# Optimization experiments

Measured on AMD Instinct MI355X. Metric: run time of the kernel, lower is better.

## Reference

```python
import math
import jax, jax.numpy as jnp
import numpy as np

DIM = 2048
HID = 4 * DIM
SEQ = 2048
BATCH = 2
EPS = 1e-5


def _layernorm(x, g, b):
    mu = jnp.mean(x, axis=-1, keepdims=True)
    var = jnp.var(x, axis=-1, keepdims=True)
    return (x - mu) * jax.lax.rsqrt(var + EPS) * g + b


def setup_inputs() -> dict:
    key = jax.random.key(0)
    ks = jax.random.split(key, 12)
    s = 1.0 / math.sqrt(DIM)
    x = jax.random.normal(ks[0], (BATCH, SEQ, DIM), dtype=jnp.float32)
    # additive causal mask: 0 on/below diagonal, -1e9 above
    mask = jnp.where(jnp.tril(jnp.ones((SEQ, SEQ), dtype=bool)), 0.0, -1e9).astype(jnp.float32)
    freqs_cis = jax.random.normal(ks[1], (SEQ, 64), dtype=jnp.float32)  # unused by forward
    return {
        "x": x,
        "mask": mask,
        "start_pos": 0,
        "freqs_cis": freqs_cis,
        "wq": jax.random.normal(ks[2], (DIM, DIM), dtype=jnp.float32) * s,
        "bq": jnp.zeros((DIM,), dtype=jnp.float32),
        "wk": jax.random.normal(ks[3], (DIM, DIM), dtype=jnp.float32) * s,
        "bk": jnp.zeros((DIM,), dtype=jnp.float32),
        "wv": jax.random.normal(ks[4], (DIM, DIM), dtype=jnp.float32) * s,
        "bv": jnp.zeros((DIM,), dtype=jnp.float32),
        "g_ln1": jnp.ones((DIM,), dtype=jnp.float32),
        "b_ln1": jnp.zeros((DIM,), dtype=jnp.float32),
        "g_ln2": jnp.ones((DIM,), dtype=jnp.float32),
        "b_ln2": jnp.zeros((DIM,), dtype=jnp.float32),
        "w1": jax.random.normal(ks[5], (DIM, HID), dtype=jnp.float32) * s,
        "b1": jnp.zeros((HID,), dtype=jnp.float32),
        "w2": jax.random.normal(ks[6], (HID, DIM), dtype=jnp.float32) * (1.0 / math.sqrt(HID)),
        "b2": jnp.zeros((DIM,), dtype=jnp.float32),
    }


def reference(x, mask, start_pos, freqs_cis, wq, bq, wk, bk, wv, bv,
              g_ln1, b_ln1, g_ln2, b_ln2, w1, b1, w2, b2):
    # pre-norm attention (no head split; scale by sqrt(full dim); dropout=eval identity)
    h = _layernorm(x, g_ln1, b_ln1)
    q = h @ wq + bq
    k = h @ wk + bk
    v = h @ wv + bv
    scores = jnp.einsum('bqd,bkd->bqk', q, k) / math.sqrt(DIM) + mask
    attn = jax.nn.softmax(scores, axis=-1)
    attn_out = jnp.einsum('bqk,bkd->bqd', attn, v)
    h2 = _layernorm(x + attn_out, g_ln2, b_ln2)
    ffn = jax.nn.gelu(h2 @ w1 + b1, approximate=False) @ w2 + b2
    # NOTE: original code adds FFN output to the ORIGINAL x (attn residual dropped here)
    return x + ffn
```

## Files before the change

### kernel.cpp

```cpp
#include <hip/hip_runtime.h>
#include <math.h>

#define DIM_ 2048
#define HID_ 8192
#define SEQ_ 2048
#define BATCH_ 2
#define TOK_ (BATCH_*SEQ_)

typedef __attribute__((ext_vector_type(4))) float f32x4;
typedef __attribute__((ext_vector_type(8))) __bf16 bf16x8;
typedef __attribute__((ext_vector_type(4))) unsigned int u32x4;
typedef __attribute__((ext_vector_type(4))) short s16x4;
typedef __attribute__((ext_vector_type(8))) short s16x8;
typedef __attribute__((address_space(3))) short* lds_sp;

__device__ __forceinline__ short f2bf(float f) {
  union { float f; unsigned u; } v; v.f = f;
  unsigned r = v.u + 0x7FFFu + ((v.u >> 16) & 1u);
  return (short)(r >> 16);
}
__device__ __forceinline__ float bf2f(short s) {
  union { unsigned u; float f; } v; v.u = ((unsigned)(unsigned short)s) << 16;
  return v.f;
}

__device__ __forceinline__ f32x4 mfma16(u32x4 a, u32x4 b, f32x4 c) {
  return __builtin_amdgcn_mfma_f32_16x16x32_bf16(
      __builtin_bit_cast(bf16x8, a), __builtin_bit_cast(bf16x8, b), c, 0, 0, 0);
}

#define DSR(dst, addr) asm volatile("ds_read_b128 %0, %1" : "=v"(dst) : "v"(addr))
#define BARv()  __builtin_amdgcn_s_barrier()
#define LGKMW(n) do { asm volatile("s_waitcnt lgkmcnt(" #n ")" ::: "memory"); \
                      __builtin_amdgcn_sched_barrier(0); } while(0)
#define VM3()   asm volatile("s_waitcnt vmcnt(3)" ::: "memory")
#define VM4()   asm volatile("s_waitcnt vmcnt(4)" ::: "memory")
#define PRIO1() __builtin_amdgcn_s_setprio(1)
#define PRIO0() __builtin_amdgcn_s_setprio(0)
#define AS1 const __attribute__((address_space(1))) void*
#define AS3 __attribute__((address_space(3))) void*

#define TILE_MAP(BM, BN) \
  const int nwg  = gridDim.x * gridDim.y; \
  const int orig = blockIdx.y * gridDim.x + blockIdx.x; \
  const int wgid = (orig & 7) * (nwg >> 3) + (orig >> 3); \
  const int gy4  = (int)gridDim.y << 2; \
  const int rem  = wgid % gy4; \
  const int tn   = ((wgid / gy4) * 4 + (rem & 3)) * (BN); \
  const int tm   = (rem >> 2) * (BM);

template<int EPI>
__device__ __forceinline__ void epi_store(void* Cv, const float* bias, const float* aux,
                                          int z, long long sC, int ldc, int N,
                                          int row, int col, float v)
{
  if (EPI == 1) {
    ((float*)Cv + (long long)z * sC)[(long long)row * ldc + col] = v;
  } else if (EPI == 0) {
    v += bias[col];
    ((short*)Cv + (long long)z * sC)[(long long)row * ldc + col] = f2bf(v);
  } else if (EPI == 2) {
    v += bias[col];
    v = 0.5f * v * (1.0f + erff(v * 0.70710678118654752f));
    ((short*)Cv + (long long)z * sC)[(long long)row * ldc + col] = f2bf(v);
  } else if (EPI == 3) {
    v += bias[col] + aux[(long long)row * ldc + col];
    ((float*)Cv + (long long)z * sC)[(long long)row * ldc + col] = v;
  } else {
    v = v * 0.022097086912079608f + aux[(long long)row * ldc + col];
    ((short*)Cv + (long long)z * sC)[(long long)row * ldc + col] = f2bf(v);
  }
}

#define G256_RD1(slot) do { \
  const unsigned s_ = (unsigned)(slot)*16384u; \
  DSR(af[0], aRd + s_);          DSR(af[1], aRd + s_ + 1024u); \
  DSR(af[2], aRd + s_ + 2048u);  DSR(af[3], aRd + s_ + 3072u); \
  DSR(af[4], aRd + s_ + 4096u);  DSR(af[5], aRd + s_ + 5120u); \
  DSR(af[6], aRd + s_ + 6144u);  DSR(af[7], aRd + s_ + 7168u); \
  DSR(bf0[0], bRd + s_);         DSR(bf0[1], bRd + s_ + 1024u); \
} while(0)

#define G256_RD2(slot) do { \
  const unsigned s_ = (unsigned)(slot)*16384u; \
  DSR(bf1[0], bRd + s_ + 2048u); DSR(bf1[1], bRd + s_ + 3072u); \
} while(0)

#define G256_MM(c0, bA, bB) do { \
  _Pragma("unroll") \
  for (int fr_ = 0; fr_ < 8; ++fr_) { \
    acc[fr_][(c0)]   = mfma16(af[fr_], bA, acc[fr_][(c0)]); \
    acc[fr_][(c0)+1] = mfma16(af[fr_], bB, acc[fr_][(c0)+1]); \
  } \
} while(0)

template<int EPI>
__global__ __launch_bounds__(512, 2)
void gemm256(const short* __restrict__ A, const short* __restrict__ B,
             void* __restrict__ Cv, const float* __restrict__ bias,
             const float* __restrict__ aux,
             int M, int N, int K, int lda, int ldb, int ldc,
             long long sA, long long sB, long long sC)
{
  __shared__ __align__(16) short As[3*256*32];
  __shared__ __align__(16) short Bs[3*256*32];
  const int lane = threadIdx.x & 63;
  const int wave = threadIdx.x >> 6;
  const int wr = wave >> 2, wc = wave & 3;
  TILE_MAP(256, 256)
  const int z = blockIdx.z;
  A += (long long)z * sA;
  B += (long long)z * sB;

  const int NT = K >> 5;

  const int rr   = wave * 16 + (lane >> 2);
  const int soff = (((lane & 3) ^ ((lane >> 3) & 3)) << 3);
  const short* pA = A + (long long)(tm + rr) * lda + soff;
  const short* pB = B + (long long)(tn + rr) * ldb + soff;
  const long long lda128 = 128LL * lda;
  const long long ldb128 = 128LL * ldb;

  auto stA = [&](int t, int slot) {
    const long long ko = (long long)t << 5;
    __builtin_amdgcn_global_load_lds((AS1)(pA + ko),
        (AS3)(As + slot * 8192 + wave * 512), 16, 0, 0);
    __builtin_amdgcn_global_load_lds((AS1)(pA + lda128 + ko),
        (AS3)(As + slot * 8192 + 4096 + wave * 512), 16, 0, 0);
  };
  auto stB = [&](int t, int slot) {
    const long long ko = (long long)t << 5;
    __builtin_amdgcn_global_load_lds((AS1)(pB + ko),
        (AS3)(Bs + slot * 8192 + wave * 512), 16, 0, 0);
    __builtin_amdgcn_global_load_lds((AS1)(pB + ldb128 + ko),
        (AS3)(Bs + slot * 8192 + 4096 + wave * 512), 16, 0, 0);
  };

  const unsigned asB = (unsigned)(unsigned long long)(lds_sp)As;
  const unsigned bsB = (unsigned)(unsigned long long)(lds_sp)Bs;
  const int l15 = lane & 15, l4 = lane >> 4;
  const unsigned offk = (unsigned)((l4 ^ ((l15 >> 1) & 3)) << 4);
  const unsigned aRd = asB + (unsigned)((wr * 128 + l15) * 64) + offk;
  const unsigned bRd = bsB + (unsigned)((wc * 64 + l15) * 64) + offk;

  f32x4 acc[8][4] = {};
  u32x4 af[8], bf0[2], bf1[2];

  stA(0, 0); stB(0, 0);
  stA(1 < NT ? 1 : 0, 1); stB(1 < NT ? 1 : 0, 1);
  VM4();
  BARv();

  int rd = 0;
  #pragma unroll 1
  for (int t = 0; t < NT; ++t) {
    const int st = rd + 2 >= 3 ? rd - 1 : rd + 2;
    const int tc = t + 2 < NT ? t + 2 : NT - 1;
    G256_RD1(rd);
    G256_RD2(rd);
    stA(tc, st); stB(tc, st);
    LGKMW(2);
    PRIO1(); G256_MM(0, bf0[0], bf0[1]);
    LGKMW(0);
    G256_MM(2, bf1[0], bf1[1]); PRIO0();
    VM4();
    BARv();
    rd = rd + 1 >= 3 ? 0 : rd + 1;
  }

  const int row0 = tm + wr * 128 + l4 * 4;
  const int col0 = tn + wc * 64 + l15;
  #pragma unroll
  for (int fr = 0; fr < 8; ++fr)
    #pragma unroll
    for (int j = 0; j < 4; ++j)
      #pragma unroll
      for (int fc = 0; fc < 4; ++fc)
        epi_store<EPI>(Cv, bias, aux, z, sC, ldc, N,
                       row0 + fr * 16 + j, col0 + fc * 16, acc[fr][fc][j]);
}

template<int EPI>
__global__ __launch_bounds__(512, 2)
void gemm_bn128(const short* __restrict__ A, const short* __restrict__ B,
                void* __restrict__ Cv, const float* __restrict__ bias,
                const float* __restrict__ aux,
                int M, int N, int K, int lda, int ldb, int ldc,
                long long sA, long long sB, long long sC)
{
  __shared__ __align__(16) short As[3*256*32];
  __shared__ __align__(16) short Bs[3*256*32];
  const int lane = threadIdx.x & 63;
  const int wave = threadIdx.x >> 6;
  const int wr = wave >> 2, wc = wave & 3;
  TILE_MAP(256, 128)
  const int z = blockIdx.z;
  A += (long long)z * sA;
  B += (long long)z * sB;

  const int NT = K >> 5;

  const int rr   = wave * 16 + (lane >> 2);
  const int soff = (((lane & 3) ^ ((lane >> 3) & 3)) << 3);
  const short* pA = A + (long long)(tm + rr) * lda + soff;
  const short* pB = B + (long long)(tn + rr) * ldb + soff;
  const long long lda128 = 128LL * lda;

  auto stage = [&](int t, int slot) {
    const long long ko = (long long)t << 5;
    __builtin_amdgcn_global_load_lds((AS1)(pA + ko),
        (AS3)(As + slot * 8192 + wave * 512), 16, 0, 0);
    __builtin_amdgcn_global_load_lds((AS1)(pA + lda128 + ko),
        (AS3)(As + slot * 8192 + 4096 + wave * 512), 16, 0, 0);
    __builtin_amdgcn_global_load_lds((AS1)(pB + ko),
        (AS3)(Bs + slot * 8192 + wave * 512), 16, 0, 0);
  };

  const unsigned asB = (unsigned)(unsigned long long)(lds_sp)As;
  const unsigned bsB = (unsigned)(unsigned long long)(lds_sp)Bs;
  const int l15 = lane & 15, l4 = lane >> 4;
  const unsigned offk = (unsigned)((l4 ^ ((l15 >> 1) & 3)) << 4);
  const unsigned aRd = asB + (unsigned)((wr * 128 + l15) * 64) + offk;
  const unsigned bRd = bsB + (unsigned)((wc * 32 + l15) * 64) + offk;

  f32x4 acc[8][2] = {};
  u32x4 af[8], bf[2];

  stage(0, 0);
  stage(1 < NT ? 1 : 0, 1);
  VM3();
  BARv();

  int rd = 0;
  #pragma unroll 1
  for (int t = 0; t < NT; ++t) {
    const int st = rd + 2 >= 3 ? rd - 1 : rd + 2;
    const int tc = t + 2 < NT ? t + 2 : NT - 1;
    {
      const unsigned s_ = (unsigned)rd * 16384u;
      DSR(bf[0], bRd + s_);          DSR(bf[1], bRd + s_ + 1024u);
      DSR(af[0], aRd + s_);          DSR(af[1], aRd + s_ + 1024u);
      DSR(af[2], aRd + s_ + 2048u);  DSR(af[3], aRd + s_ + 3072u);
      DSR(af[4], aRd + s_ + 4096u);  DSR(af[5], aRd + s_ + 5120u);
      DSR(af[6], aRd + s_ + 6144u);  DSR(af[7], aRd + s_ + 7168u);
    }
    stage(tc, st);
    LGKMW(4);
    PRIO1();
    #pragma unroll
    for (int fr = 0; fr < 4; ++fr) {
      acc[fr][0] = mfma16(af[fr], bf[0], acc[fr][0]);
      acc[fr][1] = mfma16(af[fr], bf[1], acc[fr][1]);
    }
    LGKMW(0);
    #pragma unroll
    for (int fr = 4; fr < 8; ++fr) {
      acc[fr][0] = mfma16(af[fr], bf[0], acc[fr][0]);
      acc[fr][1] = mfma16(af[fr], bf[1], acc[fr][1]);
    }
    PRIO0();
    VM3();
    BARv();
    rd = rd + 1 >= 3 ? 0 : rd + 1;
  }

  const int row0 = tm + wr * 128 + l4 * 4;
  const int col0 = tn + wc * 32 + l15;
  #pragma unroll
  for (int fr = 0; fr < 8; ++fr)
    #pragma unroll
    for (int j = 0; j < 4; ++j)
      #pragma unroll
      for (int fc = 0; fc < 2; ++fc)
        epi_store<EPI>(Cv, bias, aux, z, sC, ldc, N,
                       row0 + fr * 16 + j, col0 + fc * 16, acc[fr][fc][j]);
}

#define HRD2(slot) do { \
  const unsigned a_ = aBaseH + (unsigned)(slot)*8192u; \
  const unsigned b_ = bBaseH + (unsigned)(slot)*16384u; \
  DSR(bf[0], b_ + offk);          DSR(bf[1], b_ + 1024u + offk); \
  DSR(bf[2], b_ + 2048u + offk);  DSR(bf[3], b_ + 3072u + offk); \
  DSR(af[0], a_ + offk);          DSR(af[1], a_ + 1024u + offk); \
  DSR(af[2], a_ + 2048u + offk);  DSR(af[3], a_ + 3072u + offk); \
} while(0)

#define HROW(mi) do { \
  _Pragma("unroll") \
  for (int ni = 0; ni < 4; ++ni) \
    acc[mi][ni] = mfma16(af[mi], bf[ni], acc[mi][ni]); \
} while(0)

template<int EPI, int CZ>
__global__ __launch_bounds__(512, 4)
void gemm_hi(const short* __restrict__ A, const short* __restrict__ B,
             void* __restrict__ Cv, const float* __restrict__ bias,
             const float* __restrict__ aux,
             int M, int N, int K, int lda, int ldb, int ldc,
             long long sA, long long sB, long long sC)
{
  __shared__ __align__(16) short As[3*128*32];
  __shared__ __align__(16) short Bs[3*256*32];
  const int lane = threadIdx.x & 63;
  const int wave = threadIdx.x >> 6;
  const int wr = wave >> 2, wc = wave & 3;
  TILE_MAP(128, 256)
  if (CZ == 1 && tn >= tm + 128) return;
  const int z = blockIdx.z;
  A += (long long)z * sA;
  B += (long long)z * sB;

  const int NT = (CZ == 2) ? ((tm + 128) >> 5) : (K >> 5);

  const int rr   = wave * 16 + (lane >> 2);
  const int soff = (((lane & 3) ^ ((lane >> 3) & 3)) << 3);
  const short* pA = A + (long long)(tm + rr) * lda + soff;
  const short* pB = B + (long long)(tn + rr) * ldb + soff;
  const long long ldb128 = 128LL * ldb;

  auto stage = [&](int t, int slot) {
    const long long ko = (long long)t << 5;
    __builtin_amdgcn_global_load_lds((AS1)(pA + ko),
        (AS3)(As + slot * 4096 + wave * 512), 16, 0, 0);
    __builtin_amdgcn_global_load_lds((AS1)(pB + ko),
        (AS3)(Bs + slot * 8192 + wave * 512), 16, 0, 0);
    __builtin_amdgcn_global_load_lds((AS1)(pB + ldb128 + ko),
        (AS3)(Bs + slot * 8192 + 4096 + wave * 512), 16, 0, 0);
  };

  const unsigned asB = (unsigned)(unsigned long long)(lds_sp)As;
  const unsigned bsB = (unsigned)(unsigned long long)(lds_sp)Bs;
  const int l15 = lane & 15, l4 = lane >> 4;
  const unsigned offk  = (unsigned)((l4 ^ ((l15 >> 1) & 3)) << 4);
  const unsigned aBaseH = asB + (unsigned)(wr * 4096 + l15 * 64);
  const unsigned bBaseH = bsB + (unsigned)(wc * 4096 + l15 * 64);

  f32x4 acc[4][4] = {};
  u32x4 af[4], bf[4];

  stage(0, 0);
  stage(1 < NT ? 1 : 0, 1);
  VM3();
  BARv();

  int rd = 0;
  #pragma unroll 1
  for (int t = 0; t < NT; ++t) {
    const int st = rd + 2 >= 3 ? rd - 1 : rd + 2;
    const int tc = t + 2 < NT ? t + 2 : NT - 1;
    HRD2(rd);
    stage(tc, st);
    LGKMW(3);
    PRIO1(); HROW(0);
    LGKMW(2); HROW(1);
    LGKMW(1); HROW(2);
    LGKMW(0); HROW(3); PRIO0();
    VM3();
    BARv();
    rd = rd + 1 >= 3 ? 0 : rd + 1;
  }

  const int row0 = tm + wr * 64 + l4 * 4;
  const int col0 = tn + wc * 64 + l15;
  #pragma unroll
  for (int mi = 0; mi < 4; ++mi)
    #pragma unroll
    for (int j = 0; j < 4; ++j)
      #pragma unroll
      for (int ni = 0; ni < 4; ++ni)
        epi_store<EPI>(Cv, bias, aux, z, sC, ldc, N,
                       row0 + mi * 16 + j, col0 + ni * 16, acc[mi][ni][j]);
}

__global__ __launch_bounds__(256)
void ln_kernel(const float* __restrict__ x, const float* __restrict__ res,
               const float* __restrict__ g, const float* __restrict__ b,
               short* __restrict__ out, int hasres)
{
  const int row = blockIdx.x;
  const int tid = threadIdx.x;
  const float4* X = (const float4*)x + (long long)row * 512;
  float4 v0 = X[tid], v1 = X[tid + 256];
  if (hasres) {
    const float4* R = (const float4*)res + (long long)row * 512;
    float4 r0 = R[tid], r1 = R[tid + 256];
    v0.x += r0.x; v0.y += r0.y; v0.z += r0.z; v0.w += r0.w;
    v1.x += r1.x; v1.y += r1.y; v1.z += r1.z; v1.w += r1.w;
  }
  float s1 = v0.x + v0.y + v0.z + v0.w + v1.x + v1.y + v1.z + v1.w;
  float s2 = v0.x*v0.x + v0.y*v0.y + v0.z*v0.z + v0.w*v0.w
           + v1.x*v1.x + v1.y*v1.y + v1.z*v1.z + v1.w*v1.w;
  #pragma unroll
  for (int o = 32; o > 0; o >>= 1) { s1 += __shfl_xor(s1, o); s2 += __shfl_xor(s2, o); }
  __shared__ float red[8];
  if ((tid & 63) == 0) { red[tid >> 6] = s1; red[4 + (tid >> 6)] = s2; }
  __syncthreads();
  s1 = red[0] + red[1] + red[2] + red[3];
  s2 = red[4] + red[5] + red[6] + red[7];
  const float mean = s1 * (1.0f / 2048.0f);
  const float var  = s2 * (1.0f / 2048.0f) - mean * mean;
  const float rstd = rsqrtf(var + 1e-5f);
  const float4* G  = (const float4*)g;
  const float4* Bb = (const float4*)b;
  float4 g0 = G[tid], g1 = G[tid + 256], b0 = Bb[tid], b1 = Bb[tid + 256];
  s16x4 o0, o1;
  o0[0] = f2bf((v0.x - mean) * rstd * g0.x + b0.x);
  o0[1] = f2bf((v0.y - mean) * rstd * g0.y + b0.y);
  o0[2] = f2bf((v0.z - mean) * rstd * g0.z + b0.z);
  o0[3] = f2bf((v0.w - mean) * rstd * g0.w + b0.w);
  o1[0] = f2bf((v1.x - mean) * rstd * g1.x + b1.x);
  o1[1] = f2bf((v1.y - mean) * rstd * g1.y + b1.y);
  o1[2] = f2bf((v1.z - mean) * rstd * g1.z + b1.z);
  o1[3] = f2bf((v1.w - mean) * rstd * g1.w + b1.w);
  *(s16x4*)&out[(long long)row * 2048 + tid * 4]        = o0;
  *(s16x4*)&out[(long long)row * 2048 + 1024 + tid * 4] = o1;
}

__global__ __launch_bounds__(256)
void softmax_causal_kernel(short* __restrict__ probs)
{
  const long long row = blockIdx.x;
  const int q  = blockIdx.x & (SEQ_ - 1);
  const int tid = threadIdx.x;
  short* P = probs + row * 2048 + tid * 8;
  const int kbase = tid * 8;
  s16x8 in = *(const s16x8*)P;
  float a[8];
  #pragma unroll
  for (int i = 0; i < 8; ++i) a[i] = bf2f(in[i]);
  float mx = -1e30f;
  #pragma unroll
  for (int i = 0; i < 8; ++i) {
    const float av = (kbase + i <= q) ? a[i] : -1e30f;
    mx = fmaxf(mx, av);
  }
  #pragma unroll
  for (int o = 32; o > 0; o >>= 1) mx = fmaxf(mx, __shfl_xor(mx, o));
  __shared__ float red[8];
  if ((tid & 63) == 0) red[tid >> 6] = mx;
  __syncthreads();
  mx = fmaxf(fmaxf(red[0], red[1]), fmaxf(red[2], red[3]));
  float e[8], sum = 0.f;
  #pragma unroll
  for (int i = 0; i < 8; ++i) {
    e[i] = (kbase + i <= q) ? __expf(a[i] - mx) : 0.f;
    sum += e[i];
  }
  #pragma unroll
  for (int o = 32; o > 0; o >>= 1) sum += __shfl_xor(sum, o);
  if ((tid & 63) == 0) red[4 + (tid >> 6)] = sum;
  __syncthreads();
  sum = red[4] + red[5] + red[6] + red[7];
  const float inv = 1.0f / sum;
  s16x8 o;
  #pragma unroll
  for (int i = 0; i < 8; ++i) o[i] = f2bf(e[i] * inv);
  *(s16x8*)P = o;
}

__global__ __launch_bounds__(256)
void cvt_transpose64(const float* __restrict__ in, short* __restrict__ out,
                     int R, int C)
{
  __shared__ float t[64][69];
  const int r0 = blockIdx.y << 6, c0 = blockIdx.x << 6;
  const int tx = threadIdx.x & 15, ty = threadIdx.x >> 4;
  #pragma unroll
  for (int p = 0; p < 4; ++p) {
    const int r = ty + p * 16;
    float4 v = *(const float4*)&in[(long long)(r0 + r) * C + c0 + tx * 4];
    t[r][tx*4+0] = v.x; t[r][tx*4+1] = v.y; t[r][tx*4+2] = v.z; t[r][tx*4+3] = v.w;
  }
  __syncthreads();
  #pragma unroll
  for (int p = 0; p < 4; ++p) {
    const int oc = ty + p * 16;
    s16x4 o;
    o[0] = f2bf(t[tx*4+0][oc]); o[1] = f2bf(t[tx*4+1][oc]);
    o[2] = f2bf(t[tx*4+2][oc]); o[3] = f2bf(t[tx*4+3][oc]);
    *(s16x4*)&out[(long long)(c0 + oc) * R + r0 + tx * 4] = o;
  }
}

__global__ __launch_bounds__(256)
void transpose_bf16_kernel(const short* __restrict__ in, short* __restrict__ out,
                           int ldin, int ldout, long long sin_, long long sout_)
{
  __shared__ short t[32][33];
  in  += (long long)blockIdx.z * sin_;
  out += (long long)blockIdx.z * sout_;
  const int tx = threadIdx.x & 31, ty = threadIdx.x >> 5;
  const int r0 = blockIdx.y << 5, c0 = blockIdx.x << 5;
  #pragma unroll
  for (int i = 0; i < 32; i += 8)
    t[ty + i][tx] = in[(long long)(r0 + ty + i) * ldin + c0 + tx];
  __syncthreads();
  #pragma unroll
  for (int i = 0; i < 32; i += 8)
    out[(long long)(c0 + ty + i) * ldout + r0 + tx] = t[tx][ty + i];
}

__global__ __launch_bounds__(256)
void concat_bias_kernel(const float* a, const float* b, const float* c, float* o)
{
  const int i = blockIdx.x * 256 + threadIdx.x;
  o[i] = i < 2048 ? a[i] : (i < 4096 ? b[i - 2048] : c[i - 4096]);
}

extern "C" void kernel_launch(void* const* d_in, const int* in_sizes, int n_in,
                              void* d_out, int out_size, void* d_ws, size_t ws_size,
                              hipStream_t stream)
{
  const float* x    = (const float*)d_in[0];
  const float* mask = (const float*)d_in[1];
  const float* wq   = (const float*)d_in[4];
  const float* bq   = (const float*)d_in[5];
  const float* wk   = (const float*)d_in[6];
  const float* bk   = (const float*)d_in[7];
  const float* wv   = (const float*)d_in[8];
  const float* bv   = (const float*)d_in[9];
  const float* g1   = (const float*)d_in[10];
  const float* b1   = (const float*)d_in[11];
  const float* g2   = (const float*)d_in[12];
  const float* b2   = (const float*)d_in[13];
  const float* w1   = (const float*)d_in[14];
  const float* bw1  = (const float*)d_in[15];
  const float* w2   = (const float*)d_in[16];
  const float* bw2  = (const float*)d_in[17];
  float* out = (float*)d_out;

  char* p = (char*)d_ws;
  auto take = [&](size_t bytes) { char* r = p; p += (bytes + 255) & ~(size_t)255; return r; };
  short* wqkvT = (short*)take((size_t)3 * DIM_ * DIM_ * 2);
  short* w1T   = (short*)take((size_t)DIM_ * HID_ * 2);
  short* w2T   = (short*)take((size_t)HID_ * DIM_ * 2);
  short* h_bf  = (short*)take((size_t)TOK_ * DIM_ * 2);
  short* qkv   = (short*)take((size_t)TOK_ * 3 * DIM_ * 2);
  short* vT    = (short*)take((size_t)BATCH_ * DIM_ * SEQ_ * 2);
  float* attno = (float*)take((size_t)TOK_ * DIM_ * 4);
  short* attn  = (short*)take((size_t)BATCH_ * SEQ_ * SEQ_ * 2);
  float* cbias = (float*)take((size_t)3 * DIM_ * 4);
  short* ffn1  = qkv;
  short* h2    = h_bf;

  const dim3 blk(256), gblk(512);
  cvt_transpose64<<<dim3(DIM_/64, DIM_/64), blk, 0, stream>>>(wq, wqkvT, DIM_, DIM_);
  cvt_transpose64<<<dim3(DIM_/64, DIM_/64), blk, 0, stream>>>(wk, wqkvT + (size_t)DIM_*DIM_, DIM_, DIM_);
  cvt_transpose64<<<dim3(DIM_/64, DIM_/64), blk, 0, stream>>>(wv, wqkvT + (size_t)2*DIM_*DIM_, DIM_, DIM_);
  cvt_transpose64<<<dim3(HID_/64, DIM_/64), blk, 0, stream>>>(w1, w1T, DIM_, HID_);
  cvt_transpose64<<<dim3(DIM_/64, HID_/64), blk, 0, stream>>>(w2, w2T, HID_, DIM_);
  concat_bias_kernel<<<24, blk, 0, stream>>>(bq, bk, bv, cbias);
  ln_kernel<<<TOK_, blk, 0, stream>>>(x, nullptr, g1, b1, h_bf, 0);
  gemm_bn128<0><<<dim3(6144/128, TOK_/256, 1), gblk, 0, stream>>>(
      h_bf, wqkvT, qkv, cbias, nullptr, TOK_, 6144, DIM_, DIM_, DIM_, 6144, 0, 0, 0);
  gemm_hi<4,1><<<dim3(SEQ_/256, SEQ_/128, BATCH_), gblk, 0, stream>>>(
      qkv, qkv + DIM_, attn, nullptr, mask, SEQ_, SEQ_, DIM_, 6144, 6144, SEQ_,
      (long long)SEQ_ * 6144, (long long)SEQ_ * 6144, (long long)SEQ_ * SEQ_);
  softmax_causal_kernel<<<BATCH_ * SEQ_, blk, 0, stream>>>(attn);
  transpose_bf16_kernel<<<dim3(DIM_/32, SEQ_/32, BATCH_), blk, 0, stream>>>(
      qkv + 2*DIM_, vT, 6144, SEQ_, (long long)SEQ_ * 6144, (long long)DIM_ * SEQ_);
  gemm_hi<1,2><<<dim3(DIM_/256, SEQ_/128, BATCH_), gblk, 0, stream>>>(
      attn, vT, attno, nullptr, nullptr, SEQ_, DIM_, SEQ_, SEQ_, SEQ_, DIM_,
      (long long)SEQ_ * SEQ_, (long long)DIM_ * SEQ_, (long long)SEQ_ * DIM_);
  ln_kernel<<<TOK_, blk, 0, stream>>>(x, attno, g2, b2, h2, 1);
  gemm256<2><<<dim3(HID_/256, TOK_/256, 1), gblk, 0, stream>>>(
      h2, w1T, ffn1, bw1, nullptr, TOK_, HID_, DIM_, DIM_, DIM_, HID_, 0, 0, 0);
  gemm_hi<3,0><<<dim3(DIM_/256, TOK_/128, 1), gblk, 0, stream>>>(
      ffn1, w2T, out, bw2, x, TOK_, DIM_, HID_, HID_, HID_, DIM_, 0, 0, 0);
}
```

Baseline: 621.8 us.

## Switch GEMMs to 4-slot double-tile pipeline, bf16 attention output, fused QKV weight convert

The gemm256 and gemm_bn128 kernels move from a 3-slot ring with a barrier per K-tile to a 4-slot ring that processes two K-tiles per barrier and waits on vmcnt(0). A new gemm_hi4 kernel uses the same scheme for the FFN down-projection. The attention-output GEMM now writes bf16 through a new epilogue, and layernorm 2 reads that bf16 residual, halving that buffer's traffic at some precision cost. The three Q/K/V weight conversion launches are merged into one 3D launch. Halving the barriers targets synchronisation overhead, but the larger LDS footprint and full vmcnt drains may reduce occupancy or overlap.

```diff
diff --git a/kernel.cpp b/kernel.cpp
--- a/kernel.cpp
+++ b/kernel.cpp
@@ -33,8 +33,8 @@
 #define BARv()  __builtin_amdgcn_s_barrier()
 #define LGKMW(n) do { asm volatile("s_waitcnt lgkmcnt(" #n ")" ::: "memory"); \
                       __builtin_amdgcn_sched_barrier(0); } while(0)
+#define VM0()   asm volatile("s_waitcnt vmcnt(0)" ::: "memory")
 #define VM3()   asm volatile("s_waitcnt vmcnt(3)" ::: "memory")
-#define VM4()   asm volatile("s_waitcnt vmcnt(4)" ::: "memory")
 #define PRIO1() __builtin_amdgcn_s_setprio(1)
 #define PRIO0() __builtin_amdgcn_s_setprio(0)
 #define AS1 const __attribute__((address_space(1))) void*
@@ -66,8 +66,10 @@
   } else if (EPI == 3) {
     v += bias[col] + aux[(long long)row * ldc + col];
     ((float*)Cv + (long long)z * sC)[(long long)row * ldc + col] = v;
+  } else if (EPI == 4) {
+    v = v * 0.022097086912079608f + aux[(long long)row * ldc + col];
+    ((short*)Cv + (long long)z * sC)[(long long)row * ldc + col] = f2bf(v);
   } else {
-    v = v * 0.022097086912079608f + aux[(long long)row * ldc + col];
     ((short*)Cv + (long long)z * sC)[(long long)row * ldc + col] = f2bf(v);
   }
 }
@@ -94,6 +96,15 @@
   } \
 } while(0)
 
+#define G256_TILE(slot, tt, sslot) do { \
+  G256_RD1(slot); G256_RD2(slot); \
+  stA(tt, sslot); stB(tt, sslot); \
+  LGKMW(2); \
+  PRIO1(); G256_MM(0, bf0[0], bf0[1]); \
+  LGKMW(0); \
+  G256_MM(2, bf1[0], bf1[1]); PRIO0(); \
+} while(0)
+
 template<int EPI>
 __global__ __launch_bounds__(512, 2)
 void gemm256(const short* __restrict__ A, const short* __restrict__ B,
@@ -102,8 +113,8 @@
              int M, int N, int K, int lda, int ldb, int ldc,
              long long sA, long long sB, long long sC)
 {
-  __shared__ __align__(16) short As[3*256*32];
-  __shared__ __align__(16) short Bs[3*256*32];
+  __shared__ __align__(16) short As[4*256*32];
+  __shared__ __align__(16) short Bs[4*256*32];
   const int lane = threadIdx.x & 63;
   const int wave = threadIdx.x >> 6;
   const int wr = wave >> 2, wc = wave & 3;
@@ -113,6 +124,7 @@
   B += (long long)z * sB;
 
   const int NT = K >> 5;
+  const int NW = NT >> 1;
 
   const int rr   = wave * 16 + (lane >> 2);
   const int soff = (((lane & 3) ^ ((lane >> 3) & 3)) << 3);
@@ -148,24 +160,20 @@
 
   stA(0, 0); stB(0, 0);
   stA(1 < NT ? 1 : 0, 1); stB(1 < NT ? 1 : 0, 1);
-  VM4();
+  VM0();
   BARv();
 
   int rd = 0;
   #pragma unroll 1
-  for (int t = 0; t < NT; ++t) {
-    const int st = rd + 2 >= 3 ? rd - 1 : rd + 2;
-    const int tc = t + 2 < NT ? t + 2 : NT - 1;
-    G256_RD1(rd);
-    G256_RD2(rd);
-    stA(tc, st); stB(tc, st);
-    LGKMW(2);
-    PRIO1(); G256_MM(0, bf0[0], bf0[1]);
-    LGKMW(0);
-    G256_MM(2, bf1[0], bf1[1]); PRIO0();
-    VM4();
+  for (int w = 0; w < NW; ++w) {
+    const int t2 = 2*w + 2 < NT ? 2*w + 2 : NT - 1;
+    const int t3 = 2*w + 3 < NT ? 2*w + 3 : NT - 1;
+    const int st = rd ^ 2;
+    G256_TILE(rd,     t2, st);
+    G256_TILE(rd + 1, t3, st + 1);
+    VM0();
     BARv();
-    rd = rd + 1 >= 3 ? 0 : rd + 1;
+    rd ^= 2;
   }
 
   const int row0 = tm + wr * 128 + l4 * 4;
@@ -180,6 +188,30 @@
                        row0 + fr * 16 + j, col0 + fc * 16, acc[fr][fc][j]);
 }
 
+#define BN128_TILE(slot, tt, sslot) do { \
+  const unsigned s_ = (unsigned)(slot)*16384u; \
+  DSR(bf[0], bRd + s_);          DSR(bf[1], bRd + s_ + 1024u); \
+  DSR(af[0], aRd + s_);          DSR(af[1], aRd + s_ + 1024u); \
+  DSR(af[2], aRd + s_ + 2048u);  DSR(af[3], aRd + s_ + 3072u); \
+  DSR(af[4], aRd + s_ + 4096u);  DSR(af[5], aRd + s_ + 5120u); \
+  DSR(af[6], aRd + s_ + 6144u);  DSR(af[7], aRd + s_ + 7168u); \
+  stage(tt, sslot); \
+  LGKMW(4); \
+  PRIO1(); \
+  _Pragma("unroll") \
+  for (int fr_ = 0; fr_ < 4; ++fr_) { \
+    acc[fr_][0] = mfma16(af[fr_], bf[0], acc[fr_][0]); \
+    acc[fr_][1] = mfma16(af[fr_], bf[1], acc[fr_][1]); \
+  } \
+  LGKMW(0); \
+  _Pragma("unroll") \
+  for (int fr_ = 4; fr_ < 8; ++fr_) { \
+    acc[fr_][0] = mfma16(af[fr_], bf[0], acc[fr_][0]); \
+    acc[fr_][1] = mfma16(af[fr_], bf[1], acc[fr_][1]); \
+  } \
+  PRIO0(); \
+} while(0)
+
 template<int EPI>
 __global__ __launch_bounds__(512, 2)
 void gemm_bn128(const short* __restrict__ A, const short* __restrict__ B,
@@ -188,8 +220,8 @@
                 int M, int N, int K, int lda, int ldb, int ldc,
                 long long sA, long long sB, long long sC)
 {
-  __shared__ __align__(16) short As[3*256*32];
-  __shared__ __align__(16) short Bs[3*256*32];
+  __shared__ __align__(16) short As[4*256*32];
+  __shared__ __align__(16) short Bs[4*128*32];
   const int lane = threadIdx.x & 63;
   const int wave = threadIdx.x >> 6;
   const int wr = wave >> 2, wc = wave & 3;
@@ -199,6 +231,7 @@
   B += (long long)z * sB;
 
   const int NT = K >> 5;
+  const int NW = NT >> 1;
 
   const int rr   = wave * 16 + (lane >> 2);
   const int soff = (((lane & 3) ^ ((lane >> 3) & 3)) << 3);
@@ -213,7 +246,7 @@
     __builtin_amdgcn_global_load_lds((AS1)(pA + lda128 + ko),
         (AS3)(As + slot * 8192 + 4096 + wave * 512), 16, 0, 0);
     __builtin_amdgcn_global_load_lds((AS1)(pB + ko),
-        (AS3)(Bs + slot * 8192 + wave * 512), 16, 0, 0);
+        (AS3)(Bs + slot * 4096 + wave * 512), 16, 0, 0);
   };
 
   const unsigned asB = (unsigned)(unsigned long long)(lds_sp)As;
@@ -221,47 +254,80 @@
   const int l15 = lane & 15, l4 = lane >> 4;
   const unsigned offk = (unsigned)((l4 ^ ((l15 >> 1) & 3)) << 4);
   const unsigned aRd = asB + (unsigned)((wr * 128 + l15) * 64) + offk;
-  const unsigned bRd = bsB + (unsigned)((wc * 32 + l15) * 64) + offk;
+  const unsigned bRd0 = bsB + (unsigned)((wc * 32 + l15) * 64) + offk;
 
   f32x4 acc[8][2] = {};
   u32x4 af[8], bf[2];
 
   stage(0, 0);
   stage(1 < NT ? 1 : 0, 1);
-  VM3();
+  VM0();
   BARv();
 
   int rd = 0;
   #pragma unroll 1
-  for (int t = 0; t < NT; ++t) {
-    const int st = rd + 2 >= 3 ? rd - 1 : rd + 2;
-    const int tc = t + 2 < NT ? t + 2 : NT - 1;
+  for (int w = 0; w < NW; ++w) {
+    const int t2 = 2*w + 2 < NT ? 2*w + 2 : NT - 1;
+    const int t3 = 2*w + 3 < NT ? 2*w + 3 : NT - 1;
+    const int st = rd ^ 2;
     {
-      const unsigned s_ = (unsigned)rd * 16384u;
-      DSR(bf[0], bRd + s_);          DSR(bf[1], bRd + s_ + 1024u);
-      DSR(af[0], aRd + s_);          DSR(af[1], aRd + s_ + 1024u);
-      DSR(af[2], aRd + s_ + 2048u);  DSR(af[3], aRd + s_ + 3072u);
-      DSR(af[4], aRd + s_ + 4096u);  DSR(af[5], aRd + s_ + 5120u);
-      DSR(af[6], aRd + s_ + 6144u);  DSR(af[7], aRd + s_ + 7168u);
+      const unsigned bRd = bRd0 - (unsigned)0;
+      {
+        const unsigned s_ = (unsigned)rd * 8192u;
+        DSR(bf[0], bRd0 + s_);          DSR(bf[1], bRd0 + s_ + 1024u);
+      }
+      {
+        const unsigned s_ = (unsigned)rd * 16384u;
+        DSR(af[0], aRd + s_);          DSR(af[1], aRd + s_ + 1024u);
+        DSR(af[2], aRd + s_ + 2048u);  DSR(af[3], aRd + s_ + 3072u);
+        DSR(af[4], aRd + s_ + 4096u);  DSR(af[5], aRd + s_ + 5120u);
+        DSR(af[6], aRd + s_ + 6144u);  DSR(af[7], aRd + s_ + 7168u);
+      }
+      stage(t2, st);
+      LGKMW(4);
+      PRIO1();
+      #pragma unroll
+      for (int fr = 0; fr < 4; ++fr) {
+        acc[fr][0] = mfma16(af[fr], bf[0], acc[fr][0]);
+        acc[fr][1] = mfma16(af[fr], bf[1], acc[fr][1]);
+      }
+      LGKMW(0);
+      #pragma unroll
+      for (int fr = 4; fr < 8; ++fr) {
+        acc[fr][0] = mfma16(af[fr], bf[0], acc[fr][0]);
+        acc[fr][1] = mfma16(af[fr], bf[1], acc[fr][1]);
+      }
+      PRIO0();
+      {
+        const unsigned s_ = (unsigned)(rd + 1) * 8192u;
+        DSR(bf[0], bRd0 + s_);          DSR(bf[1], bRd0 + s_ + 1024u);
+      }
+      {
+        const unsigned s_ = (unsigned)(rd + 1) * 16384u;
+        DSR(af[0], aRd + s_);          DSR(af[1], aRd + s_ + 1024u);
+        DSR(af[2], aRd + s_ + 2048u);  DSR(af[3], aRd + s_ + 3072u);
+        DSR(af[4], aRd + s_ + 4096u);  DSR(af[5], aRd + s_ + 5120u);
+        DSR(af[6], aRd + s_ + 6144u);  DSR(af[7], aRd + s_ + 7168u);
+      }
+      stage(t3, st + 1);
+      LGKMW(4);
+      PRIO1();
+      #pragma unroll
+      for (int fr = 0; fr < 4; ++fr) {
+        acc[fr][0] = mfma16(af[fr], bf[0], acc[fr][0]);
+        acc[fr][1] = mfma16(af[fr], bf[1], acc[fr][1]);
+      }
+      LGKMW(0);
+      #pragma unroll
+      for (int fr = 4; fr < 8; ++fr) {
+        acc[fr][0] = mfma16(af[fr], bf[0], acc[fr][0]);
+        acc[fr][1] = mfma16(af[fr], bf[1], acc[fr][1]);
+      }
+      PRIO0();
     }
-    stage(tc, st);
-    LGKMW(4);
-    PRIO1();
-    #pragma unroll
-    for (int fr = 0; fr < 4; ++fr) {
-      acc[fr][0] = mfma16(af[fr], bf[0], acc[fr][0]);
-      acc[fr][1] = mfma16(af[fr], bf[1], acc[fr][1]);
-    }
-    LGKMW(0);
-    #pragma unroll
-    for (int fr = 4; fr < 8; ++fr) {
-      acc[fr][0] = mfma16(af[fr], bf[0], acc[fr][0]);
-      acc[fr][1] = mfma16(af[fr], bf[1], acc[fr][1]);
-    }
-    PRIO0();
-    VM3();
+    VM0();
     BARv();
-    rd = rd + 1 >= 3 ? 0 : rd + 1;
+    rd ^= 2;
   }
 
   const int row0 = tm + wr * 128 + l4 * 4;
@@ -372,8 +438,100 @@
                        row0 + mi * 16 + j, col0 + ni * 16, acc[mi][ni][j]);
 }
 
+#define H4_TILE(slot, tt, sslot) do { \
+  const unsigned a_ = aBaseH + (unsigned)(slot)*8192u; \
+  const unsigned b_ = bBaseH + (unsigned)(slot)*16384u; \
+  DSR(bf[0], b_ + offk);          DSR(bf[1], b_ + 1024u + offk); \
+  DSR(bf[2], b_ + 2048u + offk);  DSR(bf[3], b_ + 3072u + offk); \
+  DSR(af[0], a_ + offk);          DSR(af[1], a_ + 1024u + offk); \
+  DSR(af[2], a_ + 2048u + offk);  DSR(af[3], a_ + 3072u + offk); \
+  stage(tt, sslot); \
+  LGKMW(3); \
+  PRIO1(); HROW(0); \
+  LGKMW(2); HROW(1); \
+  LGKMW(1); HROW(2); \
+  LGKMW(0); HROW(3); PRIO0(); \
+} while(0)
+
+template<int EPI>
+__global__ __launch_bounds__(512, 2)
+void gemm_hi4(const short* __restrict__ A, const short* __restrict__ B,
+              void* __restrict__ Cv, const float* __restrict__ bias,
+              const float* __restrict__ aux,
+              int M, int N, int K, int lda, int ldb, int ldc,
+              long long sA, long long sB, long long sC)
+{
+  __shared__ __align__(16) short As[4*128*32];
+  __shared__ __align__(16) short Bs[4*256*32];
+  const int lane = threadIdx.x & 63;
+  const int wave = threadIdx.x >> 6;
+  const int wr = wave >> 2, wc = wave & 3;
+  TILE_MAP(128, 256)
+  const int z = blockIdx.z;
+  A += (long long)z * sA;
+  B += (long long)z * sB;
+
+  const int NT = K >> 5;
+  const int NW = NT >> 1;
+
+  const int rr   = wave * 16 + (lane >> 2);
+  const int soff = (((lane & 3) ^ ((lane >> 3) & 3)) << 3);
+  const short* pA = A + (long long)(tm + rr) * lda + soff;
+  const short* pB = B + (long long)(tn + rr) * ldb + soff;
+  const long long ldb128 = 128LL * ldb;
+
+  auto stage = [&](int t, int slot) {
+    const long long ko = (long long)t << 5;
+    __builtin_amdgcn_global_load_lds((AS1)(pA + ko),
+        (AS3)(As + slot * 4096 + wave * 512), 16, 0, 0);
+    __builtin_amdgcn_global_load_lds((AS1)(pB + ko),
+        (AS3)(Bs + slot * 8192 + wave * 512), 16, 0, 0);
+    __builtin_amdgcn_global_load_lds((AS1)(pB + ldb128 + ko),
+        (AS3)(Bs + slot * 8192 + 4096 + wave * 512), 16, 0, 0);
+  };
+
+  const unsigned asB = (unsigned)(unsigned long long)(lds_sp)As;
+  const unsigned bsB = (unsigned)(unsigned long long)(lds_sp)Bs;
+  const int l15 = lane & 15, l4 = lane >> 4;
+  const unsigned offk  = (unsigned)((l4 ^ ((l15 >> 1) & 3)) << 4);
+  const unsigned aBaseH = asB + (unsigned)(wr * 4096 + l15 * 64);
+  const unsigned bBaseH = bsB + (unsigned)(wc * 4096 + l15 * 64);
+
+  f32x4 acc[4][4] = {};
+  u32x4 af[4], bf[4];
+
+  stage(0, 0);
+  stage(1 < NT ? 1 : 0, 1);
+  VM0();
+  BARv();
+
+  int rd = 0;
+  #pragma unroll 1
+  for (int w = 0; w < NW; ++w) {
+    const int t2 = 2*w + 2 < NT ? 2*w + 2 : NT - 1;
+    const int t3 = 2*w + 3 < NT ? 2*w + 3 : NT - 1;
+    const int st = rd ^ 2;
+    H4_TILE(rd,     t2, st);
+    H4_TILE(rd + 1, t3, st + 1);
+    VM0();
+    BARv();
+    rd ^= 2;
+  }
+
+  const int row0 = tm + wr * 64 + l4 * 4;
+  const int col0 = tn + wc * 64 + l15;
+  #pragma unroll
+  for (int mi = 0; mi < 4; ++mi)
+    #pragma unroll
+    for (int j = 0; j < 4; ++j)
+      #pragma unroll
+      for (int ni = 0; ni < 4; ++ni)
+        epi_store<EPI>(Cv, bias, aux, z, sC, ldc, N,
+                       row0 + mi * 16 + j, col0 + ni * 16, acc[mi][ni][j]);
+}
+
 __global__ __launch_bounds__(256)
-void ln_kernel(const float* __restrict__ x, const float* __restrict__ res,
+void ln_kernel(const float* __restrict__ x, const void* __restrict__ res,
                const float* __restrict__ g, const float* __restrict__ b,
                short* __restrict__ out, int hasres)
 {
@@ -381,11 +539,17 @@
   const int tid = threadIdx.x;
   const float4* X = (const float4*)x + (long long)row * 512;
   float4 v0 = X[tid], v1 = X[tid + 256];
-  if (hasres) {
+  if (hasres == 1) {
     const float4* R = (const float4*)res + (long long)row * 512;
     float4 r0 = R[tid], r1 = R[tid + 256];
     v0.x += r0.x; v0.y += r0.y; v0.z += r0.z; v0.w += r0.w;
     v1.x += r1.x; v1.y += r1.y; v1.z += r1.z; v1.w += r1.w;
+  } else if (hasres == 2) {
+    const short* R = (const short*)res + (long long)row * 2048;
+    s16x4 r0 = *(const s16x4*)&R[tid * 4];
+    s16x4 r1 = *(const s16x4*)&R[1024 + tid * 4];
+    v0.x += bf2f(r0[0]); v0.y += bf2f(r0[1]); v0.z += bf2f(r0[2]); v0.w += bf2f(r0[3]);
+    v1.x += bf2f(r1[0]); v1.y += bf2f(r1[1]); v1.z += bf2f(r1[2]); v1.w += bf2f(r1[3]);
   }
   float s1 = v0.x + v0.y + v0.z + v0.w + v1.x + v1.y + v1.z + v1.w;
   float s2 = v0.x*v0.x + v0.y*v0.y + v0.z*v0.z + v0.w*v0.w
@@ -458,9 +622,7 @@
   *(s16x8*)P = o;
 }
 
-__global__ __launch_bounds__(256)
-void cvt_transpose64(const float* __restrict__ in, short* __restrict__ out,
-                     int R, int C)
+__device__ __forceinline__ void cvt_t64_body(const float* in, short* out, int R, int C)
 {
   __shared__ float t[64][69];
   const int r0 = blockIdx.y << 6, c0 = blockIdx.x << 6;
@@ -480,6 +642,20 @@
     o[2] = f2bf(t[tx*4+2][oc]); o[3] = f2bf(t[tx*4+3][oc]);
     *(s16x4*)&out[(long long)(c0 + oc) * R + r0 + tx * 4] = o;
   }
+}
+
+__global__ __launch_bounds__(256)
+void cvt_transpose64(const float* __restrict__ in, short* __restrict__ out,
+                     int R, int C)
+{ cvt_t64_body(in, out, R, C); }
+
+__global__ __launch_bounds__(256)
+void cvt3_transpose64(const float* __restrict__ a, const float* __restrict__ b,
+                      const float* __restrict__ c, short* __restrict__ out)
+{
+  const int z = blockIdx.z;
+  const float* in = z == 0 ? a : (z == 1 ? b : c);
+  cvt_t64_body(in, out + (size_t)z * DIM_ * DIM_, DIM_, DIM_);
 }
 
 __global__ __launch_bounds__(256)
@@ -537,16 +713,14 @@
   short* h_bf  = (short*)take((size_t)TOK_ * DIM_ * 2);
   short* qkv   = (short*)take((size_t)TOK_ * 3 * DIM_ * 2);
   short* vT    = (short*)take((size_t)BATCH_ * DIM_ * SEQ_ * 2);
-  float* attno = (float*)take((size_t)TOK_ * DIM_ * 4);
+  short* attno = (short*)take((size_t)TOK_ * DIM_ * 2);
   short* attn  = (short*)take((size_t)BATCH_ * SEQ_ * SEQ_ * 2);
   float* cbias = (float*)take((size_t)3 * DIM_ * 4);
   short* ffn1  = qkv;
   short* h2    = h_bf;
 
   const dim3 blk(256), gblk(512);
-  cvt_transpose64<<<dim3(DIM_/64, DIM_/64), blk, 0, stream>>>(wq, wqkvT, DIM_, DIM_);
-  cvt_transpose64<<<dim3(DIM_/64, DIM_/64), blk, 0, stream>>>(wk, wqkvT + (size_t)DIM_*DIM_, DIM_, DIM_);
-  cvt_transpose64<<<dim3(DIM_/64, DIM_/64), blk, 0, stream>>>(wv, wqkvT + (size_t)2*DIM_*DIM_, DIM_, DIM_);
+  cvt3_transpose64<<<dim3(DIM_/64, DIM_/64, 3), blk, 0, stream>>>(wq, wk, wv, wqkvT);
   cvt_transpose64<<<dim3(HID_/64, DIM_/64), blk, 0, stream>>>(w1, w1T, DIM_, HID_);
   cvt_transpose64<<<dim3(DIM_/64, HID_/64), blk, 0, stream>>>(w2, w2T, HID_, DIM_);
   concat_bias_kernel<<<24, blk, 0, stream>>>(bq, bk, bv, cbias);
@@ -559,12 +733,12 @@
   softmax_causal_kernel<<<BATCH_ * SEQ_, blk, 0, stream>>>(attn);
   transpose_bf16_kernel<<<dim3(DIM_/32, SEQ_/32, BATCH_), blk, 0, stream>>>(
       qkv + 2*DIM_, vT, 6144, SEQ_, (long long)SEQ_ * 6144, (long long)DIM_ * SEQ_);
-  gemm_hi<1,2><<<dim3(DIM_/256, SEQ_/128, BATCH_), gblk, 0, stream>>>(
+  gemm_hi<5,2><<<dim3(DIM_/256, SEQ_/128, BATCH_), gblk, 0, stream>>>(
       attn, vT, attno, nullptr, nullptr, SEQ_, DIM_, SEQ_, SEQ_, SEQ_, DIM_,
       (long long)SEQ_ * SEQ_, (long long)DIM_ * SEQ_, (long long)SEQ_ * DIM_);
-  ln_kernel<<<TOK_, blk, 0, stream>>>(x, attno, g2, b2, h2, 1);
+  ln_kernel<<<TOK_, blk, 0, stream>>>(x, attno, g2, b2, h2, 2);
   gemm256<2><<<dim3(HID_/256, TOK_/256, 1), gblk, 0, stream>>>(
       h2, w1T, ffn1, bw1, nullptr, TOK_, HID_, DIM_, DIM_, DIM_, HID_, 0, 0, 0);
-  gemm_hi<3,0><<<dim3(DIM_/256, TOK_/128, 1), gblk, 0, stream>>>(
+  gemm_hi4<3><<<dim3(DIM_/256, TOK_/128, 1), gblk, 0, stream>>>(
       ffn1, w2T, out, bw2, x, TOK_, DIM_, HID_, HID_, HID_, DIM_, 0, 0, 0);
 }
```

New measurement: 645.7 us. 1.04x slower.
